# Optimization experiments

Hardware: AMD Instinct MI355X
Metric: run time of the kernel (lower is better)

## Reference

```python
import jax, jax.numpy as jnp
from jax import lax
import numpy as np
from math import sqrt

B, S, H = 64, 512, 2048
RHO = 0.8


def setup_inputs() -> dict:
    key = jax.random.key(0)
    ks = jax.random.split(key, 6)
    x = jax.random.normal(ks[0], (B, S, 1), dtype=jnp.float32)
    noise = jax.random.normal(ks[1], (B, S, H), dtype=jnp.float32)
    wi_flat = jax.random.normal(ks[2], (H, 1), dtype=jnp.float32)
    wo = jax.random.normal(ks[3], (H, 1), dtype=jnp.float32)
    A = jax.random.normal(ks[4], (H, 1), dtype=jnp.float32)
    A = A / jnp.linalg.norm(A)
    rec_noise = jax.random.normal(ks[5], (H, H), dtype=jnp.float32) * (RHO / sqrt(H))
    overlap_wi = jnp.ones((1,), dtype=jnp.float32)
    overlap_wo = jnp.ones((1,), dtype=jnp.float32)
    overlap_mn = jnp.ones((1,), dtype=jnp.float32)
    h0 = jnp.zeros((H,), dtype=jnp.float32)
    return {"x": x, "noise": noise, "wi_flat": wi_flat, "wo": wo, "A": A,
            "rec_noise": rec_noise, "overlap_wi": overlap_wi,
            "overlap_wo": overlap_wo, "overlap_mn": overlap_mn, "h0": h0}


def reference(x, noise, wi_flat, wo, A, rec_noise, overlap_wi, overlap_wo, overlap_mn, h0):
    noise_std = 0.05
    alpha = 0.2
    hidden = wi_flat.shape[0]
    batch = x.shape[0]
    hf = jnp.float32(hidden)

    # rank-one structured recurrent connectivity + fixed noise matrix
    n_rec = overlap_wi * hf / jnp.sum(wi_flat ** 2) * wi_flat + jnp.sqrt(overlap_mn * hf) * A  # [H,1]
    m_rec = overlap_wo * hf / jnp.sum(wo ** 2) * wo + jnp.sqrt(overlap_mn * hf) * A            # [H,1]
    w_rec = (n_rec @ m_rec.T) / hf + rec_noise  # [H,H]
    wi_row = wi_flat.reshape(1, hidden)          # [1,H]

    h_init = jnp.broadcast_to(h0, (batch, hidden))
    r_init = jnp.tanh(h_init)

    xs = (jnp.swapaxes(x, 0, 1), jnp.swapaxes(noise, 0, 1))  # [S,B,1], [S,B,H]

    def step(carry, inp):
        h, r = carry
        x_t, n_t = inp
        h = h + noise_std * n_t + alpha * (-h + r @ w_rec + x_t @ wi_row)
        r = jnp.tanh(h)
        out_t = r @ wo / hf  # [B,1]
        return (h, r), out_t

    _, outs = lax.scan(step, (h_init, r_init), xs)  # [S,B,1]
    return jnp.swapaxes(outs, 0, 1)  # [B,S,1]
```

## Files before the change

### kernel.cpp

```cpp
#include <hip/hip_runtime.h>
#include <math.h>

#define BATCH 64
#define SEQ   512
#define HID   2048
#define NT    320
#define NBLK  256

typedef float f4 __attribute__((ext_vector_type(4)));

__device__ __forceinline__ float gload(const float* p) {
    return __hip_atomic_load(p, __ATOMIC_RELAXED, __HIP_MEMORY_SCOPE_AGENT);
}
__device__ __forceinline__ void gstore(float* p, float v) {
    __hip_atomic_store(p, v, __ATOMIC_RELAXED, __HIP_MEMORY_SCOPE_AGENT);
}
__device__ __forceinline__ unsigned gloadu(const unsigned* p) {
    return __hip_atomic_load(p, __ATOMIC_RELAXED, __HIP_MEMORY_SCOPE_AGENT);
}
__device__ __forceinline__ void gstoreu(unsigned* p, unsigned v) {
    __hip_atomic_store(p, v, __ATOMIC_RELAXED, __HIP_MEMORY_SCOPE_AGENT);
}

__device__ __forceinline__ void gbar(unsigned t, unsigned* arrive,
                                     unsigned* epoch, int bid, int tid) {
    asm volatile("s_waitcnt vmcnt(0)" ::: "memory");
    __syncthreads();
    if (bid == 0) {
        if (tid > 0 && tid < NBLK) {
            while (gloadu(&arrive[tid]) != t) __builtin_amdgcn_s_sleep(1);
        }
        __syncthreads();
        if (tid == 0) gstoreu(epoch, t);
        __syncthreads();
    } else {
        if (tid == 0) {
            gstoreu(&arrive[bid], t);
            while (gloadu(epoch) != t) __builtin_amdgcn_s_sleep(1);
        }
        __syncthreads();
    }
}

extern __shared__ float lds[];

__global__ void __launch_bounds__(NT, 1)
rnn_kernel(const float* __restrict__ x,
           const float* __restrict__ noise,
           const float* __restrict__ wi,
           const float* __restrict__ wo,
           const float* __restrict__ Av,
           const float* __restrict__ rn,
           const float* __restrict__ ovwi,
           const float* __restrict__ ovwo,
           const float* __restrict__ ovmn,
           const float* __restrict__ h0,
           float* __restrict__ out,
           float* __restrict__ ws)
{
    const int tid  = threadIdx.x;
    const int bid  = blockIdx.x;
    const int w    = tid >> 6;
    const int lane = tid & 63;
    const int ks = lane & 7;
    const int bg = lane >> 3;
    const int jU = tid & 7;
    const int b1 = tid >> 3;
    const int b2 = b1 + 32;
    const int cb = ((bid & 7) << 5) | (bid >> 3);
    const int jB = cb*8 + jU;

    float* wsm  = lds;
    float* redw = lds + HID*8;

    float* rg  = ws;
    float* ps  = rg + 2*HID*BATCH;
    float* po  = ps + 2*BATCH*NBLK;
    float* sS  = po + 2*BATCH*NBLK;
    float* red = sS + 64;
    unsigned* flags      = (unsigned*)(red + NBLK*16);
    unsigned* bar_arrive = flags + 8;
    unsigned* bar_epoch  = bar_arrive + NBLK + 56;
    unsigned bt = 0;

    {
        const f4* rn4 = (const f4*)rn;
        f4* wsm4 = (f4*)wsm;
        #pragma unroll
        for (int u = 0; u < 16; ++u) {
            if (tid < 256) {
                int idx = u*256 + tid;
                int k = idx >> 1, half = idx & 1;
                wsm4[idx] = rn4[(size_t)k*512 + cb*2 + half];
            }
        }
    }

    float pwi = 0.f, pwo = 0.f;
    for (int i = tid; i < HID; i += NT) {
        float a = wi[i]; pwi = fmaf(a, a, pwi);
        float c = wo[i]; pwo = fmaf(c, c, pwo);
    }
    #pragma unroll
    for (int m = 32; m >= 1; m >>= 1) { pwi += __shfl_xor(pwi, m, 64); pwo += __shfl_xor(pwo, m, 64); }
    if (lane == 0) { gstore(&red[bid*16 + w], pwi); gstore(&red[bid*16 + 8 + w], pwo); }

    const float wiB = wi[jB], woB = wo[jB], aB = Av[jB];
    float h_1 = h0[jB];
    float h_2 = h_1;
    float r_1 = tanhf(h_1), r_2 = r_1;
    if (tid < 256) {
        gstore(&rg[jB*BATCH + b1], r_1);
        gstore(&rg[jB*BATCH + b2], r_2);
        float q1 = r_1*woB, q2 = r_2*woB;
        #pragma unroll
        for (int m = 4; m >= 1; m >>= 1) { q1 += __shfl_xor(q1, m, 8); q2 += __shfl_xor(q2, m, 8); }
        if (jU == 0) { gstore(&po[b1*NBLK + bid], q1); gstore(&po[b2*NBLK + bid], q2); }
    }
    gbar(++bt, bar_arrive, bar_epoch, bid, tid);

    float s_wi = 0.f, s_wo = 0.f;
    #pragma unroll
    for (int i2 = 0; i2 < 5; ++i2) { s_wi += gload(&red[bid*16 + i2]); s_wo += gload(&red[bid*16 + 8 + i2]); }
    const float hf = (float)HID, inv_hf = 1.0f/hf;
    const float c_mn = sqrtf(ovmn[0]*hf);
    const float nB = fmaf(ovwi[0]*hf/s_wi, wiB, c_mn*aB);
    const float mB = fmaf(ovwo[0]*hf/s_wo, woB, c_mn*aB);
    const float mi = mB*inv_hf;
    if (tid < 256) {
        float p1 = r_1*nB, p2 = r_2*nB;
        #pragma unroll
        for (int m = 4; m >= 1; m >>= 1) { p1 += __shfl_xor(p1, m, 8); p2 += __shfl_xor(p2, m, 8); }
        if (jU == 0) { gstore(&ps[b1*NBLK + bid], p1); gstore(&ps[b2*NBLK + bid], p2); }
    }
    gbar(++bt, bar_arrive, bar_epoch, bid, tid);

    const int rb1 = (b1 & ~7)*8 + (((b1 & 7) ^ (b1 >> 3)) & 7)*8 + jU;
    const int rb2 = (b2 & ~7)*8 + (((b2 & 7) ^ (b2 >> 3)) & 7)*8 + jU;

    for (int t = 0; t <= SEQ; ++t) {
        const int pr = t & 1, pw = pr ^ 1;
        const float* rgp = rg + (size_t)pr*(HID*BATCH);

        __builtin_amdgcn_fence(__ATOMIC_ACQUIRE, "agent");

        if (w == 4 && bid < 8) {
            const int b   = bid*8 + (lane >> 3);
            const int sub = lane & 7;
            const float* psb = ps + (size_t)pr*(BATCH*NBLK) + b*NBLK;
            const float* pob = po + (size_t)pr*(BATCH*NBLK) + b*NBLK;
            float sb = 0.f, ob = 0.f;
            #pragma unroll
            for (int u = 0; u < 32; ++u) {
                sb += gload(psb + sub + u*8);
                ob += gload(pob + sub + u*8);
            }
            #pragma unroll
            for (int m = 4; m >= 1; m >>= 1) { sb += __shfl_xor(sb, m, 8); ob += __shfl_xor(ob, m, 8); }
            if (sub == 0) {
                gstore(&sS[b], sb);
                if (t > 0) out[(size_t)b*SEQ + (t-1)] = ob * inv_hf;
            }
            asm volatile("s_waitcnt vmcnt(0)" ::: "memory");
            if (lane == 0) gstoreu(&flags[bid], (unsigned)(t+1));
        }
        if (t == SEQ) break;

        float x1 = 0.f, x2 = 0.f, nz1 = 0.f, nz2 = 0.f;
        if (w < 4) {
            x1 = x[b1*SEQ + t]; x2 = x[b2*SEQ + t];
            nz1 = noise[((size_t)b1*SEQ + t)*HID + jB];
            nz2 = noise[((size_t)b2*SEQ + t)*HID + jB];

            f4 acc0[8], acc1[8];
            #pragma unroll
            for (int c = 0; c < 8; ++c) {
                acc0[c] = (f4){0.f, 0.f, 0.f, 0.f};
                acc1[c] = (f4){0.f, 0.f, 0.f, 0.f};
            }
            const float* __restrict__ rb = rgp + (size_t)(w*512 + ks)*BATCH + bg*8;
            const float* __restrict__ wb = wsm + (w*512 + ks)*8;
            #pragma unroll 4
            for (int i = 0; i < 64; ++i) {
                f4 ra0 = *(const f4*)(rb + i*512);
                f4 ra1 = *(const f4*)(rb + i*512 + 4);
                f4 wa0 = *(const f4*)(wb + i*64);
                f4 wa1 = *(const f4*)(wb + i*64 + 4);
                acc0[0] += ra0 * wa0.x; acc1[0] += ra1 * wa0.x;
                acc0[1] += ra0 * wa0.y; acc1[1] += ra1 * wa0.y;
                acc0[2] += ra0 * wa0.z; acc1[2] += ra1 * wa0.z;
                acc0[3] += ra0 * wa0.w; acc1[3] += ra1 * wa0.w;
                acc0[4] += ra0 * wa1.x; acc1[4] += ra1 * wa1.x;
                acc0[5] += ra0 * wa1.y; acc1[5] += ra1 * wa1.y;
                acc0[6] += ra0 * wa1.z; acc1[6] += ra1 * wa1.z;
                acc0[7] += ra0 * wa1.w; acc1[7] += ra1 * wa1.w;
            }
            #pragma unroll
            for (int m = 1; m <= 4; m <<= 1) {
                #pragma unroll
                for (int c = 0; c < 8; ++c) {
                    #pragma unroll
                    for (int q = 0; q < 4; ++q) {
                        acc0[c][q] += __shfl_xor(acc0[c][q], m, 64);
                        acc1[c][q] += __shfl_xor(acc1[c][q], m, 64);
                    }
                }
            }
            if (ks == 0) {
                float* dst = redw + w*512 + bg*64;
                #pragma unroll
                for (int bi = 0; bi < 4; ++bi) {
                    int slot = (bi ^ bg) & 7;
                    *(f4*)(dst + slot*8)     = (f4){acc0[0][bi], acc0[1][bi], acc0[2][bi], acc0[3][bi]};
                    *(f4*)(dst + slot*8 + 4) = (f4){acc0[4][bi], acc0[5][bi], acc0[6][bi], acc0[7][bi]};
                }
                #pragma unroll
                for (int bi = 0; bi < 4; ++bi) {
                    int slot = ((bi + 4) ^ bg) & 7;
                    *(f4*)(dst + slot*8)     = (f4){acc1[0][bi], acc1[1][bi], acc1[2][bi], acc1[3][bi]};
                    *(f4*)(dst + slot*8 + 4) = (f4){acc1[4][bi], acc1[5][bi], acc1[6][bi], acc1[7][bi]};
                }
            }
        }
        __syncthreads();

        if (tid < 256) {
            float accA = redw[rb1] + redw[512 + rb1] + redw[1024 + rb1] + redw[1536 + rb1];
            float accB = redw[rb2] + redw[512 + rb2] + redw[1024 + rb2] + redw[1536 + rb2];
            const unsigned want = (unsigned)(t + 1);
            while (gloadu(&flags[b1 >> 3]) != want) __builtin_amdgcn_s_sleep(1);
            while (gloadu(&flags[b2 >> 3]) != want) __builtin_amdgcn_s_sleep(1);
            float sb1 = gload(&sS[b1]);
            float sb2 = gload(&sS[b2]);

            float g1 = accA + sb1*mi + x1*wiB;
            float g2 = accB + sb2*mi + x2*wiB;
            h_1 += 0.05f*nz1 + 0.2f*(g1 - h_1);
            h_2 += 0.05f*nz2 + 0.2f*(g2 - h_2);
            r_1 = tanhf(h_1); r_2 = tanhf(h_2);
            float* rgw = rg + (size_t)pw*(HID*BATCH);
            gstore(&rgw[jB*BATCH + b1], r_1);
            gstore(&rgw[jB*BATCH + b2], r_2);
            float p1 = r_1*nB, p2 = r_2*nB, q1 = r_1*woB, q2 = r_2*woB;
            #pragma unroll
            for (int m = 4; m >= 1; m >>= 1) {
                p1 += __shfl_xor(p1, m, 8); p2 += __shfl_xor(p2, m, 8);
                q1 += __shfl_xor(q1, m, 8); q2 += __shfl_xor(q2, m, 8);
            }
            if (jU == 0) {
                float* psw = ps + (size_t)pw*(BATCH*NBLK);
                float* pow_ = po + (size_t)pw*(BATCH*NBLK);
                gstore(&psw[b1*NBLK + bid], p1); gstore(&psw[b2*NBLK + bid], p2);
                gstore(&pow_[b1*NBLK + bid], q1); gstore(&pow_[b2*NBLK + bid], q2);
            }
        }
        gbar(++bt, bar_arrive, bar_epoch, bid, tid);
    }
}

extern "C" void kernel_launch(void* const* d_in, const int* in_sizes, int n_in,
                              void* d_out, int out_size, void* d_ws, size_t ws_size,
                              hipStream_t stream) {
    const float* x     = (const float*)d_in[0];
    const float* noise = (const float*)d_in[1];
    const float* wi    = (const float*)d_in[2];
    const float* wo    = (const float*)d_in[3];
    const float* Av    = (const float*)d_in[4];
    const float* rn    = (const float*)d_in[5];
    const float* ovwi  = (const float*)d_in[6];
    const float* ovwo  = (const float*)d_in[7];
    const float* ovmn  = (const float*)d_in[8];
    const float* h0    = (const float*)d_in[9];
    float* out = (float*)d_out;
    float* ws  = (float*)d_ws;

    (void)hipFuncSetAttribute((const void*)rnn_kernel,
                              hipFuncAttributeMaxDynamicSharedMemorySize, 73728);

    void* args[] = { &x, &noise, &wi, &wo, &Av, &rn, &ovwi, &ovwo, &ovmn, &h0, &out, &ws };
    hipLaunchCooperativeKernel((void*)rnn_kernel, dim3(NBLK), dim3(NT),
                               args, 73728, stream);
}
```

Baseline: 14.93 ms.

## Compute rank-one projection redundantly per block to drop cross-block flag wait

Each block now keeps the full n vector in LDS and computes r·n for all batches inside its own matvec loop, rather than gathering partial sums from every block through global memory. This removes the ps partial buffer, the reduction by eight leader blocks, and the per-step spin-wait on flags, which sat in the critical path between barriers. It also moves the x and noise loads ahead of the acquire fence so they can overlap other work. The cost is a little extra FMA and shuffle work per step and more LDS per block.

```diff
diff --git a/kernel.cpp b/kernel.cpp
--- a/kernel.cpp
+++ b/kernel.cpp
@@ -72,14 +72,13 @@
 
     float* wsm  = lds;
     float* redw = lds + HID*8;
+    float* nsm  = redw + 2048;
+    float* redS = nsm + HID;
 
     float* rg  = ws;
-    float* ps  = rg + 2*HID*BATCH;
-    float* po  = ps + 2*BATCH*NBLK;
-    float* sS  = po + 2*BATCH*NBLK;
-    float* red = sS + 64;
-    unsigned* flags      = (unsigned*)(red + NBLK*16);
-    unsigned* bar_arrive = flags + 8;
+    float* po  = rg + 2*HID*BATCH;
+    float* red = po + 2*BATCH*NBLK;
+    unsigned* bar_arrive = (unsigned*)(red + NBLK*16);
     unsigned* bar_epoch  = bar_arrive + NBLK + 56;
     unsigned bt = 0;
 
@@ -124,14 +123,11 @@
     for (int i2 = 0; i2 < 5; ++i2) { s_wi += gload(&red[bid*16 + i2]); s_wo += gload(&red[bid*16 + 8 + i2]); }
     const float hf = (float)HID, inv_hf = 1.0f/hf;
     const float c_mn = sqrtf(ovmn[0]*hf);
-    const float nB = fmaf(ovwi[0]*hf/s_wi, wiB, c_mn*aB);
+    const float cwi  = ovwi[0]*hf/s_wi;
     const float mB = fmaf(ovwo[0]*hf/s_wo, woB, c_mn*aB);
     const float mi = mB*inv_hf;
-    if (tid < 256) {
-        float p1 = r_1*nB, p2 = r_2*nB;
-        #pragma unroll
-        for (int m = 4; m >= 1; m >>= 1) { p1 += __shfl_xor(p1, m, 8); p2 += __shfl_xor(p2, m, 8); }
-        if (jU == 0) { gstore(&ps[b1*NBLK + bid], p1); gstore(&ps[b2*NBLK + bid], p2); }
+    for (int k = tid; k < HID; k += NT) {
+        nsm[k] = fmaf(cwi, wi[k], c_mn*Av[k]);
     }
     gbar(++bt, bar_arrive, bar_epoch, bid, tid);
 
@@ -142,50 +138,47 @@
         const int pr = t & 1, pw = pr ^ 1;
         const float* rgp = rg + (size_t)pr*(HID*BATCH);
 
+        float x1 = 0.f, x2 = 0.f, nz1 = 0.f, nz2 = 0.f;
+        if (t < SEQ && w < 4) {
+            x1 = x[b1*SEQ + t]; x2 = x[b2*SEQ + t];
+            nz1 = noise[((size_t)b1*SEQ + t)*HID + jB];
+            nz2 = noise[((size_t)b2*SEQ + t)*HID + jB];
+        }
+
         __builtin_amdgcn_fence(__ATOMIC_ACQUIRE, "agent");
 
         if (w == 4 && bid < 8) {
             const int b   = bid*8 + (lane >> 3);
             const int sub = lane & 7;
-            const float* psb = ps + (size_t)pr*(BATCH*NBLK) + b*NBLK;
             const float* pob = po + (size_t)pr*(BATCH*NBLK) + b*NBLK;
-            float sb = 0.f, ob = 0.f;
-            #pragma unroll
-            for (int u = 0; u < 32; ++u) {
-                sb += gload(psb + sub + u*8);
-                ob += gload(pob + sub + u*8);
-            }
-            #pragma unroll
-            for (int m = 4; m >= 1; m >>= 1) { sb += __shfl_xor(sb, m, 8); ob += __shfl_xor(ob, m, 8); }
-            if (sub == 0) {
-                gstore(&sS[b], sb);
-                if (t > 0) out[(size_t)b*SEQ + (t-1)] = ob * inv_hf;
-            }
-            asm volatile("s_waitcnt vmcnt(0)" ::: "memory");
-            if (lane == 0) gstoreu(&flags[bid], (unsigned)(t+1));
+            float ob = 0.f;
+            #pragma unroll
+            for (int u = 0; u < 32; ++u) ob += gload(pob + sub + u*8);
+            #pragma unroll
+            for (int m = 4; m >= 1; m >>= 1) ob += __shfl_xor(ob, m, 8);
+            if (sub == 0 && t > 0) out[(size_t)b*SEQ + (t-1)] = ob * inv_hf;
         }
         if (t == SEQ) break;
 
-        float x1 = 0.f, x2 = 0.f, nz1 = 0.f, nz2 = 0.f;
         if (w < 4) {
-            x1 = x[b1*SEQ + t]; x2 = x[b2*SEQ + t];
-            nz1 = noise[((size_t)b1*SEQ + t)*HID + jB];
-            nz2 = noise[((size_t)b2*SEQ + t)*HID + jB];
-
             f4 acc0[8], acc1[8];
             #pragma unroll
             for (int c = 0; c < 8; ++c) {
                 acc0[c] = (f4){0.f, 0.f, 0.f, 0.f};
                 acc1[c] = (f4){0.f, 0.f, 0.f, 0.f};
             }
+            f4 sv0 = (f4){0.f, 0.f, 0.f, 0.f};
+            f4 sv1 = (f4){0.f, 0.f, 0.f, 0.f};
             const float* __restrict__ rb = rgp + (size_t)(w*512 + ks)*BATCH + bg*8;
             const float* __restrict__ wb = wsm + (w*512 + ks)*8;
+            const float* __restrict__ nsb = nsm + w*512 + ks;
             #pragma unroll 4
             for (int i = 0; i < 64; ++i) {
                 f4 ra0 = *(const f4*)(rb + i*512);
                 f4 ra1 = *(const f4*)(rb + i*512 + 4);
                 f4 wa0 = *(const f4*)(wb + i*64);
                 f4 wa1 = *(const f4*)(wb + i*64 + 4);
+                float nk = nsb[i*8];
                 acc0[0] += ra0 * wa0.x; acc1[0] += ra1 * wa0.x;
                 acc0[1] += ra0 * wa0.y; acc1[1] += ra1 * wa0.y;
                 acc0[2] += ra0 * wa0.z; acc1[2] += ra1 * wa0.z;
@@ -194,6 +187,7 @@
                 acc0[5] += ra0 * wa1.y; acc1[5] += ra1 * wa1.y;
                 acc0[6] += ra0 * wa1.z; acc1[6] += ra1 * wa1.z;
                 acc0[7] += ra0 * wa1.w; acc1[7] += ra1 * wa1.w;
+                sv0 += ra0 * nk; sv1 += ra1 * nk;
             }
             #pragma unroll
             for (int m = 1; m <= 4; m <<= 1) {
@@ -205,6 +199,11 @@
                         acc1[c][q] += __shfl_xor(acc1[c][q], m, 64);
                     }
                 }
+                #pragma unroll
+                for (int q = 0; q < 4; ++q) {
+                    sv0[q] += __shfl_xor(sv0[q], m, 64);
+                    sv1[q] += __shfl_xor(sv1[q], m, 64);
+                }
             }
             if (ks == 0) {
                 float* dst = redw + w*512 + bg*64;
@@ -220,6 +219,8 @@
                     *(f4*)(dst + slot*8)     = (f4){acc1[0][bi], acc1[1][bi], acc1[2][bi], acc1[3][bi]};
                     *(f4*)(dst + slot*8 + 4) = (f4){acc1[4][bi], acc1[5][bi], acc1[6][bi], acc1[7][bi]};
                 }
+                *(f4*)(redS + w*64 + bg*8)     = sv0;
+                *(f4*)(redS + w*64 + bg*8 + 4) = sv1;
             }
         }
         __syncthreads();
@@ -227,30 +228,24 @@
         if (tid < 256) {
             float accA = redw[rb1] + redw[512 + rb1] + redw[1024 + rb1] + redw[1536 + rb1];
             float accB = redw[rb2] + redw[512 + rb2] + redw[1024 + rb2] + redw[1536 + rb2];
-            const unsigned want = (unsigned)(t + 1);
-            while (gloadu(&flags[b1 >> 3]) != want) __builtin_amdgcn_s_sleep(1);
-            while (gloadu(&flags[b2 >> 3]) != want) __builtin_amdgcn_s_sleep(1);
-            float sb1 = gload(&sS[b1]);
-            float sb2 = gload(&sS[b2]);
-
-            float g1 = accA + sb1*mi + x1*wiB;
-            float g2 = accB + sb2*mi + x2*wiB;
+            float sA = redS[b1] + redS[64 + b1] + redS[128 + b1] + redS[192 + b1];
+            float sB = redS[b2] + redS[64 + b2] + redS[128 + b2] + redS[192 + b2];
+
+            float g1 = accA + sA*mi + x1*wiB;
+            float g2 = accB + sB*mi + x2*wiB;
             h_1 += 0.05f*nz1 + 0.2f*(g1 - h_1);
             h_2 += 0.05f*nz2 + 0.2f*(g2 - h_2);
             r_1 = tanhf(h_1); r_2 = tanhf(h_2);
             float* rgw = rg + (size_t)pw*(HID*BATCH);
             gstore(&rgw[jB*BATCH + b1], r_1);
             gstore(&rgw[jB*BATCH + b2], r_2);
-            float p1 = r_1*nB, p2 = r_2*nB, q1 = r_1*woB, q2 = r_2*woB;
+            float q1 = r_1*woB, q2 = r_2*woB;
             #pragma unroll
             for (int m = 4; m >= 1; m >>= 1) {
-                p1 += __shfl_xor(p1, m, 8); p2 += __shfl_xor(p2, m, 8);
                 q1 += __shfl_xor(q1, m, 8); q2 += __shfl_xor(q2, m, 8);
             }
             if (jU == 0) {
-                float* psw = ps + (size_t)pw*(BATCH*NBLK);
                 float* pow_ = po + (size_t)pw*(BATCH*NBLK);
-                gstore(&psw[b1*NBLK + bid], p1); gstore(&psw[b2*NBLK + bid], p2);
                 gstore(&pow_[b1*NBLK + bid], q1); gstore(&pow_[b2*NBLK + bid], q2);
             }
         }
@@ -275,9 +270,9 @@
     float* ws  = (float*)d_ws;
 
     (void)hipFuncSetAttribute((const void*)rnn_kernel,
-                              hipFuncAttributeMaxDynamicSharedMemorySize, 73728);
+                              hipFuncAttributeMaxDynamicSharedMemorySize, 82944);
 
     void* args[] = { &x, &noise, &wi, &wo, &Av, &rn, &ovwi, &ovwo, &ovmn, &h0, &out, &ws };
     hipLaunchCooperativeKernel((void*)rnn_kernel, dim3(NBLK), dim3(NT),
-                               args, 73728, stream);
-}
+                               args, 82944, stream);
+}
```

Result: faster. 14.51 ms (-2.8%).
